# Optimization experiments

Measured on AMD Instinct MI355X. Metric: run time of the kernel, lower is better.

## Reference

```python
import jax, jax.numpy as jnp
import numpy as np

B, S, D = 2, 2048, 1024
H = 16
DH = D // H  # 64


def setup_inputs() -> dict:
    key = jax.random.key(0)
    ks = jax.random.split(key, 6)
    sc = 0.02
    return {
        "x": jax.random.normal(ks[0], (B, S, D), dtype=jnp.float32),
        "Wq": jax.random.normal(ks[1], (D, D), dtype=jnp.float32) * sc,
        "Wk": jax.random.normal(ks[2], (D, D), dtype=jnp.float32) * sc,
        "Wv": jax.random.normal(ks[3], (D, D), dtype=jnp.float32) * sc,
        "Wo": jax.random.normal(ks[4], (D, D), dtype=jnp.float32) * sc,
        "bo": jnp.zeros((D,), dtype=jnp.float32),
    }


def reference(x, Wq, Wk, Wv, Wo, bo):
    b, s, _ = x.shape
    # project_qkv: Linear (x @ W.T), view to heads, transpose -> [b, H, s, DH]
    def split_heads(t):
        return t.reshape(b, s, H, DH).transpose(0, 2, 1, 3)

    q = split_heads(x @ Wq.T)
    k = split_heads(x @ Wk.T)
    v = split_heads(x @ Wv.T)

    # attn_scores = q @ k^T  [b, H, s, s]
    scores = jnp.einsum("bhqd,bhkd->bhqk", q, k)
    # causal mask: triu(ones, diagonal=1) -> mask out strictly-future positions
    causal = jnp.triu(jnp.ones((s, s), dtype=bool), k=1)
    scores = jnp.where(causal[None, None], -jnp.inf, scores)
    scale = 1.0 / jnp.sqrt(jnp.float32(DH))
    attn = jax.nn.softmax(scores * scale, axis=-1)
    # dropout p=0.0 -> identity
    ctx = jnp.einsum("bhqk,bhkd->bhqd", attn, v)
    # transpose back and flatten heads -> [b, s, D]
    ctx = ctx.transpose(0, 2, 1, 3).reshape(b, s, H * DH)
    return ctx @ Wo.T + bo
```

## Files before the change

### kernel.cpp

```cpp
#include <hip/hip_runtime.h>
#include <stdint.h>

typedef unsigned short u16;
typedef __attribute__((ext_vector_type(8))) short bf16x8;
typedef __attribute__((ext_vector_type(4))) float f32x4;
typedef __attribute__((ext_vector_type(4))) unsigned short u16x4;

__device__ __forceinline__ u16 f2bf(float f) {
  union { float f; uint32_t u; } c; c.f = f;
  uint32_t u = c.u;
  return (u16)((u + 0x7fffu + ((u >> 16) & 1u)) >> 16);
}

__device__ __forceinline__ uint32_t pk_bf16(float lo, float hi) {
  uint32_t d;
  asm("v_cvt_pk_bf16_f32 %0, %1, %2" : "=v"(d) : "v"(lo), "v"(hi));
  return d;
}

__device__ __forceinline__ void gload_lds16(const u16* g, u16* l) {
  __builtin_amdgcn_global_load_lds(
      (const __attribute__((address_space(1))) void*)g,
      (__attribute__((address_space(3))) void*)l, 16, 0, 0);
}

__global__ void cast_all(const float* __restrict__ x,
                         const float* __restrict__ Wq, const float* __restrict__ Wk,
                         const float* __restrict__ Wv, const float* __restrict__ Wo,
                         u16* __restrict__ xb, u16* __restrict__ Wcat, u16* __restrict__ Wob) {
  int i = (blockIdx.x * blockDim.x + threadIdx.x) * 4;
  const int stride = gridDim.x * blockDim.x * 4;
  for (; i < 8388608; i += stride) {
    const float* src;
    u16* dst;
    if (i < 4194304) {
      src = x + i; dst = xb + i;
    } else {
      const int j = i - 4194304;
      const int sel = j >> 20, off = j & 1048575;
      src = ((sel == 0) ? Wq : (sel == 1) ? Wk : (sel == 2) ? Wv : Wo) + off;
      dst = (sel < 3) ? (Wcat + j) : (Wob + off);
    }
    float4 v = *reinterpret_cast<const float4*>(src);
    u16x4 o = { f2bf(v.x), f2bf(v.y), f2bf(v.z), f2bf(v.w) };
    *reinterpret_cast<u16x4*>(dst) = o;
  }
}

#define QSCALE 0.18033688011112042f

template<int EPI>
__global__ __launch_bounds__(512) void gemm_bt(
    const u16* __restrict__ A, const u16* __restrict__ B,
    int M, int N, int K,
    u16* __restrict__ o0, u16* __restrict__ o1, u16* __restrict__ o2,
    float* __restrict__ fo, const float* __restrict__ bias)
{
  __shared__ __align__(16) u16 As[2][128 * 32];
  __shared__ __align__(16) u16 Bs[2][128 * 32];
  const int tid = threadIdx.x;
  const int w = tid >> 6, l = tid & 63;
  const int m0 = blockIdx.y * 128, n0 = blockIdx.x * 128;
  const int wm = w >> 1, wn = w & 1;
  const int lr = l & 15, hi = l >> 4;
  f32x4 acc[2][4] = {};

  const int ra = tid >> 2, sa = (tid & 3) ^ ((ra >> 1) & 3);
  const u16* Ap = A + (size_t)(m0 + ra) * K + sa * 8;
  const u16* Bp = B + (size_t)(n0 + ra) * K + sa * 8;

  gload_lds16(Ap, &As[0][tid * 8]);
  gload_lds16(Bp, &Bs[0][tid * 8]);

  int aoff[2], boff[4];
#pragma unroll
  for (int m = 0; m < 2; ++m) {
    const int row = wm * 32 + m * 16 + lr;
    aoff[m] = row * 64 + ((hi ^ ((row >> 1) & 3)) << 4);
  }
#pragma unroll
  for (int n = 0; n < 4; ++n) {
    const int row = wn * 64 + n * 16 + lr;
    boff[n] = row * 64 + ((hi ^ ((row >> 1) & 3)) << 4);
  }

  int buf = 0;
  for (int k0 = 0; k0 < K; k0 += 32) {
    if (k0 + 32 < K) {
      const int nb = buf ^ 1;
      gload_lds16(Ap + k0 + 32, &As[nb][tid * 8]);
      gload_lds16(Bp + k0 + 32, &Bs[nb][tid * 8]);
      asm volatile("s_waitcnt vmcnt(2)" ::: "memory");
    } else {
      asm volatile("s_waitcnt vmcnt(0)" ::: "memory");
    }
    __builtin_amdgcn_sched_barrier(0);
    __builtin_amdgcn_s_barrier();
    bf16x8 af[2], bfr[4];
#pragma unroll
    for (int m = 0; m < 2; ++m)
      af[m] = *(const bf16x8*)((const char*)&As[buf][0] + aoff[m]);
#pragma unroll
    for (int n = 0; n < 4; ++n)
      bfr[n] = *(const bf16x8*)((const char*)&Bs[buf][0] + boff[n]);
    __builtin_amdgcn_s_setprio(1);
#pragma unroll
    for (int m = 0; m < 2; ++m)
#pragma unroll
      for (int n = 0; n < 4; ++n)
        acc[m][n] = __builtin_amdgcn_mfma_f32_16x16x32_bf16(af[m], bfr[n], acc[m][n], 0, 0, 0);
    __builtin_amdgcn_s_setprio(0);
    __builtin_amdgcn_s_barrier();
    buf ^= 1;
  }

#pragma unroll
  for (int mm = 0; mm < 2; ++mm) {
#pragma unroll
    for (int nn = 0; nn < 4; ++nn) {
      const int ng = n0 + wn * 64 + nn * 16 + lr;
      if (EPI == 0) {
        const int mat = ng >> 10;
        const int col = ng & 1023;
        const int h = col >> 6, dh = col & 63;
#pragma unroll
        for (int r = 0; r < 4; ++r) {
          const int mg = m0 + wm * 32 + mm * 16 + (hi << 2) + r;
          const int b = mg >> 11, s = mg & 2047;
          if (mat == 0)
            o0[(((size_t)(b * 16 + h)) * 2048 + s) * 64 + dh] = f2bf(acc[mm][nn][r] * QSCALE);
          else if (mat == 1)
            o1[(((size_t)(b * 16 + h)) * 2048 + s) * 64 + dh] = f2bf(acc[mm][nn][r]);
          else
            o2[(((size_t)(b * 16 + h)) * 64 + dh) * 2048 + s] = f2bf(acc[mm][nn][r]);
        }
      } else {
        const float bv = bias[ng];
#pragma unroll
        for (int r = 0; r < 4; ++r) {
          const int mg = m0 + wm * 32 + mm * 16 + (hi << 2) + r;
          fo[(size_t)mg * N + ng] = acc[mm][nn][r] + bv;
        }
      }
    }
  }
}

__global__ __launch_bounds__(256) void flash_attn(
    const u16* __restrict__ Qg, const u16* __restrict__ Kg,
    const u16* __restrict__ Vtg, u16* __restrict__ ctx)
{
  __shared__ __align__(16) u16 Ks[2][4096];
  __shared__ __align__(16) u16 Vts[2][4096];
  __shared__ __align__(16) u16 PT[4][1024];
  const int tid = threadIdx.x, w = tid >> 6, l = tid & 63;
  const int lr = l & 15, hi = l >> 4;
  const int bid = blockIdx.x;
  const int xcd = bid & 7, j = bid >> 3;
  const int bh = xcd + ((j & 3) << 3);
  const int p = j >> 2;
  const size_t kqbase = (size_t)bh * (2048 * 64);
  const int h = bh & 15, b = bh >> 4;

  bf16x8 onesf;
#pragma unroll
  for (int i = 0; i < 8; ++i) onesf[i] = (short)0x3F80;

  const int c0 = w * 128 + l;
  const int c1 = c0 + 64;
  const int r0 = c0 >> 3, p0 = c0 & 7;
  const int r1 = c1 >> 3, p1 = c1 & 7;
  const u16* kg0 = Kg + kqbase + r0 * 64 + p0 * 8;
  const u16* kg1 = Kg + kqbase + r1 * 64 + p1 * 8;
  const u16* vg0 = Vtg + kqbase + (size_t)r0 * 2048 + p0 * 8;
  const u16* vg1 = Vtg + kqbase + (size_t)r1 * 2048 + p1 * 8;
  const int kw0 = (r0 << 7) + ((p0 ^ (r0 & 7)) << 4);
  const int kw1 = (r1 << 7) + ((p1 ^ (r1 & 7)) << 4);

  for (int seg = 0; seg < 2; ++seg) {
    const int qt = seg ? (31 - p) : p;
    const int q0 = qt * 64;
    const int nkt = qt + 1;
    const int qg = q0 + w * 16 + lr;

    if (seg) __builtin_amdgcn_s_barrier();

    bf16x8 qf[2];
    {
      const u16* qp = Qg + kqbase + (size_t)(q0 + w * 16 + lr) * 64 + hi * 8;
      qf[0] = *(const bf16x8*)(qp);
      qf[1] = *(const bf16x8*)(qp + 32);
    }

    f32x4 acc[4] = {};
    f32x4 acc_ls = {};

    bf16x8 sk0 = *(const bf16x8*)kg0;
    bf16x8 sk1 = *(const bf16x8*)kg1;
    bf16x8 sv0 = *(const bf16x8*)vg0;
    bf16x8 sv1 = *(const bf16x8*)vg1;
    *(bf16x8*)((char*)&Ks[0][0] + kw0) = sk0;
    *(bf16x8*)((char*)&Ks[0][0] + kw1) = sk1;
    *(bf16x8*)((char*)&Vts[0][0] + kw0) = sv0;
    *(bf16x8*)((char*)&Vts[0][0] + kw1) = sv1;
    if (nkt > 1) {
      sk0 = *(const bf16x8*)(kg0 + 4096);
      sk1 = *(const bf16x8*)(kg1 + 4096);
      sv0 = *(const bf16x8*)(vg0 + 64);
      sv1 = *(const bf16x8*)(vg1 + 64);
    }
    asm volatile("s_waitcnt lgkmcnt(0)" ::: "memory");
    __builtin_amdgcn_sched_barrier(0);
    __builtin_amdgcn_s_barrier();

    int buf = 0;
    for (int kt = 0; kt < nkt; ++kt) {
      {
        const u16* ksb = &Ks[buf][0];
        const u16* vsb = &Vts[buf][0];
        f32x4 sv[4];
        __builtin_amdgcn_s_setprio(1);
#pragma unroll
        for (int cf = 0; cf < 4; ++cf) {
          f32x4 z = {};
#pragma unroll
          for (int ch = 0; ch < 2; ++ch) {
            const int krow = cf * 16 + lr;
            const int boff = ((krow << 7) + ((ch * 32 + hi * 8) << 1)) ^ ((krow & 7) << 4);
            bf16x8 kf = *(const bf16x8*)((const char*)ksb + boff);
            z = __builtin_amdgcn_mfma_f32_16x16x32_bf16(kf, qf[ch], z, 0, 0, 0);
          }
          sv[cf] = z;
        }
        __builtin_amdgcn_s_setprio(0);

        const bool diag = (kt == nkt - 1);
        const int kb = kt * 64 + hi * 4;
#pragma unroll
        for (int cf = 0; cf < 4; ++cf) {
          f32x4 pv;
#pragma unroll
          for (int r = 0; r < 4; ++r) {
            float s = sv[cf][r];
            if (diag && (kb + cf * 16 + r) > qg) s = -1e30f;
            pv[r] = exp2f(s);
          }
          sv[cf] = pv;
        }

        {
          const int rowb = lr << 7;
          const int swz = (lr & 7) << 4;
#pragma unroll
          for (int cf = 0; cf < 4; ++cf) {
            uint32_t d0 = pk_bf16(sv[cf][0], sv[cf][1]);
            uint32_t d1 = pk_bf16(sv[cf][2], sv[cf][3]);
            uint2 val = { d0, d1 };
            const int boff = (rowb + ((cf * 16 + hi * 4) << 1)) ^ swz;
            *(uint2*)((char*)&PT[w][0] + boff) = val;
          }
        }

#pragma unroll
        for (int ch = 0; ch < 2; ++ch) {
          const int boffp = ((lr << 7) + (ch * 64 + hi * 16)) ^ ((lr & 7) << 4);
          bf16x8 pa = *(const bf16x8*)((const char*)&PT[w][0] + boffp);
          __builtin_amdgcn_s_setprio(1);
          acc_ls = __builtin_amdgcn_mfma_f32_16x16x32_bf16(pa, onesf, acc_ls, 0, 0, 0);
#pragma unroll
          for (int df = 0; df < 4; ++df) {
            const int vrow = df * 16 + lr;
            const int boffv = ((vrow << 7) + ((ch * 32 + hi * 8) << 1)) ^ ((vrow & 7) << 4);
            bf16x8 vf = *(const bf16x8*)((const char*)vsb + boffv);
            acc[df] = __builtin_amdgcn_mfma_f32_16x16x32_bf16(pa, vf, acc[df], 0, 0, 0);
          }
          __builtin_amdgcn_s_setprio(0);
        }
      }
      if (kt + 1 < nkt) {
        char* kb_ = (char*)&Ks[buf ^ 1][0];
        char* vb_ = (char*)&Vts[buf ^ 1][0];
        *(bf16x8*)(kb_ + kw0) = sk0;
        *(bf16x8*)(kb_ + kw1) = sk1;
        *(bf16x8*)(vb_ + kw0) = sv0;
        *(bf16x8*)(vb_ + kw1) = sv1;
        if (kt + 2 < nkt) {
          sk0 = *(const bf16x8*)(kg0 + (size_t)(kt + 2) * 4096);
          sk1 = *(const bf16x8*)(kg1 + (size_t)(kt + 2) * 4096);
          sv0 = *(const bf16x8*)(vg0 + (kt + 2) * 64);
          sv1 = *(const bf16x8*)(vg1 + (kt + 2) * 64);
        }
        asm volatile("s_waitcnt lgkmcnt(0)" ::: "memory");
        __builtin_amdgcn_sched_barrier(0);
        __builtin_amdgcn_s_barrier();
      }
      buf ^= 1;
    }

#pragma unroll
    for (int r = 0; r < 4; ++r) {
      const float inv = 1.0f / acc_ls[r];
      const int s = q0 + w * 16 + hi * 4 + r;
      const size_t rowbase = ((size_t)(b * 2048 + s)) * 1024 + h * 64;
#pragma unroll
      for (int df = 0; df < 4; ++df)
        ctx[rowbase + df * 16 + lr] = f2bf(acc[df][r] * inv);
    }
  }
}

extern "C" void kernel_launch(void* const* d_in, const int* in_sizes, int n_in,
                              void* d_out, int out_size, void* d_ws, size_t ws_size,
                              hipStream_t stream) {
  const float* x  = (const float*)d_in[0];
  const float* Wq = (const float*)d_in[1];
  const float* Wk = (const float*)d_in[2];
  const float* Wv = (const float*)d_in[3];
  const float* Wo = (const float*)d_in[4];
  const float* bo = (const float*)d_in[5];
  float* out = (float*)d_out;

  const size_t MB = 1ull << 20;
  if (ws_size < 48 * MB) return;
  char* ws = (char*)d_ws;
  u16* xb   = (u16*)(ws);
  u16* Wcat = (u16*)(ws + 8 * MB);
  u16* Wob  = (u16*)(ws + 14 * MB);
  u16* Qb   = (u16*)(ws + 16 * MB);
  u16* Kb   = (u16*)(ws + 24 * MB);
  u16* Vtb  = (u16*)(ws + 32 * MB);
  u16* ctxb = (u16*)(ws + 40 * MB);

  hipLaunchKernelGGL(cast_all, dim3(4096), dim3(256), 0, stream,
                     x, Wq, Wk, Wv, Wo, xb, Wcat, Wob);
  hipLaunchKernelGGL((gemm_bt<0>), dim3(24, 32), dim3(512), 0, stream,
                     xb, Wcat, 4096, 3072, 1024, Qb, Kb, Vtb, (float*)nullptr, (const float*)nullptr);
  hipLaunchKernelGGL(flash_attn, dim3(512), dim3(256), 0, stream, Qb, Kb, Vtb, ctxb);
  hipLaunchKernelGGL((gemm_bt<1>), dim3(8, 32), dim3(512), 0, stream,
                     ctxb, Wob, 4096, 1024, 1024,
                     (u16*)nullptr, (u16*)nullptr, (u16*)nullptr, out, bo);
}
```

Baseline: 117.5 us.

## Widen GEMM K-tile to 64 with register-staged prefetch and one barrier per phase

The bf16 GEMM drops direct global-to-LDS loads with a 32-wide K tile. It now uses a 64-wide K tile, staged through registers one phase ahead, with a new XOR swizzle over 8 chunks. Each phase does two MFMA sub-steps and needs only one barrier, halving barrier count and giving loads more time to overlap compute. In exchange LDS use doubles to 64KB, register pressure rises, and correctness depends on whether the compiler's waitcnt insertion covers the global loads.

Result: no change. 118.0 us (+0.5%).

```diff
diff --git a/kernel.cpp b/kernel.cpp
--- a/kernel.cpp
+++ b/kernel.cpp
@@ -56,61 +56,98 @@
     u16* __restrict__ o0, u16* __restrict__ o1, u16* __restrict__ o2,
     float* __restrict__ fo, const float* __restrict__ bias)
 {
-  __shared__ __align__(16) u16 As[2][128 * 32];
-  __shared__ __align__(16) u16 Bs[2][128 * 32];
+  __shared__ __align__(16) u16 As[2][128 * 64];
+  __shared__ __align__(16) u16 Bs[2][128 * 64];
   const int tid = threadIdx.x;
   const int w = tid >> 6, l = tid & 63;
   const int m0 = blockIdx.y * 128, n0 = blockIdx.x * 128;
   const int wm = w >> 1, wn = w & 1;
   const int lr = l & 15, hi = l >> 4;
+  const int nphase = K >> 6;
   f32x4 acc[2][4] = {};
 
-  const int ra = tid >> 2, sa = (tid & 3) ^ ((ra >> 1) & 3);
-  const u16* Ap = A + (size_t)(m0 + ra) * K + sa * 8;
-  const u16* Bp = B + (size_t)(n0 + ra) * K + sa * 8;
-
-  gload_lds16(Ap, &As[0][tid * 8]);
-  gload_lds16(Bp, &Bs[0][tid * 8]);
-
-  int aoff[2], boff[4];
+  const int ra0 = tid >> 3, sl0 = tid & 7;
+  const int ra1 = ra0 + 64, sl1 = sl0;
+  const u16* Ap0 = A + (size_t)(m0 + ra0) * K + sl0 * 8;
+  const u16* Ap1 = A + (size_t)(m0 + ra1) * K + sl1 * 8;
+  const u16* Bp0 = B + (size_t)(n0 + ra0) * K + sl0 * 8;
+  const u16* Bp1 = B + (size_t)(n0 + ra1) * K + sl1 * 8;
+  const int wb0 = (ra0 << 7) + ((sl0 ^ (ra0 & 7)) << 4);
+  const int wb1 = (ra1 << 7) + ((sl1 ^ (ra1 & 7)) << 4);
+
+  int aoff[2][2], boff[4][2];
 #pragma unroll
   for (int m = 0; m < 2; ++m) {
     const int row = wm * 32 + m * 16 + lr;
-    aoff[m] = row * 64 + ((hi ^ ((row >> 1) & 3)) << 4);
+#pragma unroll
+    for (int ch = 0; ch < 2; ++ch)
+      aoff[m][ch] = (row << 7) + (((ch * 4 + hi) ^ (row & 7)) << 4);
   }
 #pragma unroll
   for (int n = 0; n < 4; ++n) {
     const int row = wn * 64 + n * 16 + lr;
-    boff[n] = row * 64 + ((hi ^ ((row >> 1) & 3)) << 4);
-  }
+#pragma unroll
+    for (int ch = 0; ch < 2; ++ch)
+      boff[n][ch] = (row << 7) + (((ch * 4 + hi) ^ (row & 7)) << 4);
+  }
+
+  bf16x8 sa0 = *(const bf16x8*)Ap0;
+  bf16x8 sa1 = *(const bf16x8*)Ap1;
+  bf16x8 sb0 = *(const bf16x8*)Bp0;
+  bf16x8 sb1 = *(const bf16x8*)Bp1;
+  *(bf16x8*)((char*)&As[0][0] + wb0) = sa0;
+  *(bf16x8*)((char*)&As[0][0] + wb1) = sa1;
+  *(bf16x8*)((char*)&Bs[0][0] + wb0) = sb0;
+  *(bf16x8*)((char*)&Bs[0][0] + wb1) = sb1;
+  if (nphase > 1) {
+    sa0 = *(const bf16x8*)(Ap0 + 64);
+    sa1 = *(const bf16x8*)(Ap1 + 64);
+    sb0 = *(const bf16x8*)(Bp0 + 64);
+    sb1 = *(const bf16x8*)(Bp1 + 64);
+  }
+  asm volatile("s_waitcnt lgkmcnt(0)" ::: "memory");
+  __builtin_amdgcn_sched_barrier(0);
+  __builtin_amdgcn_s_barrier();
 
   int buf = 0;
-  for (int k0 = 0; k0 < K; k0 += 32) {
-    if (k0 + 32 < K) {
-      const int nb = buf ^ 1;
-      gload_lds16(Ap + k0 + 32, &As[nb][tid * 8]);
-      gload_lds16(Bp + k0 + 32, &Bs[nb][tid * 8]);
-      asm volatile("s_waitcnt vmcnt(2)" ::: "memory");
-    } else {
-      asm volatile("s_waitcnt vmcnt(0)" ::: "memory");
-    }
-    __builtin_amdgcn_sched_barrier(0);
-    __builtin_amdgcn_s_barrier();
-    bf16x8 af[2], bfr[4];
-#pragma unroll
-    for (int m = 0; m < 2; ++m)
-      af[m] = *(const bf16x8*)((const char*)&As[buf][0] + aoff[m]);
-#pragma unroll
-    for (int n = 0; n < 4; ++n)
-      bfr[n] = *(const bf16x8*)((const char*)&Bs[buf][0] + boff[n]);
-    __builtin_amdgcn_s_setprio(1);
-#pragma unroll
-    for (int m = 0; m < 2; ++m)
+  for (int kt = 0; kt < nphase; ++kt) {
+    const char* as = (const char*)&As[buf][0];
+    const char* bs = (const char*)&Bs[buf][0];
+#pragma unroll
+    for (int ch = 0; ch < 2; ++ch) {
+      bf16x8 af[2], bfr[4];
+#pragma unroll
+      for (int m = 0; m < 2; ++m)
+        af[m] = *(const bf16x8*)(as + aoff[m][ch]);
 #pragma unroll
       for (int n = 0; n < 4; ++n)
-        acc[m][n] = __builtin_amdgcn_mfma_f32_16x16x32_bf16(af[m], bfr[n], acc[m][n], 0, 0, 0);
-    __builtin_amdgcn_s_setprio(0);
-    __builtin_amdgcn_s_barrier();
+        bfr[n] = *(const bf16x8*)(bs + boff[n][ch]);
+      __builtin_amdgcn_s_setprio(1);
+#pragma unroll
+      for (int m = 0; m < 2; ++m)
+#pragma unroll
+        for (int n = 0; n < 4; ++n)
+          acc[m][n] = __builtin_amdgcn_mfma_f32_16x16x32_bf16(af[m], bfr[n], acc[m][n], 0, 0, 0);
+      __builtin_amdgcn_s_setprio(0);
+    }
+    if (kt + 1 < nphase) {
+      char* ad = (char*)&As[buf ^ 1][0];
+      char* bd = (char*)&Bs[buf ^ 1][0];
+      *(bf16x8*)(ad + wb0) = sa0;
+      *(bf16x8*)(ad + wb1) = sa1;
+      *(bf16x8*)(bd + wb0) = sb0;
+      *(bf16x8*)(bd + wb1) = sb1;
+      if (kt + 2 < nphase) {
+        const int ko = (kt + 2) * 64;
+        sa0 = *(const bf16x8*)(Ap0 + ko);
+        sa1 = *(const bf16x8*)(Ap1 + ko);
+        sb0 = *(const bf16x8*)(Bp0 + ko);
+        sb1 = *(const bf16x8*)(Bp1 + ko);
+      }
+      asm volatile("s_waitcnt lgkmcnt(0)" ::: "memory");
+      __builtin_amdgcn_sched_barrier(0);
+      __builtin_amdgcn_s_barrier();
+    }
     buf ^= 1;
   }
 
```
